# Optimization experiments

Hardware: AMD Instinct MI355X
Metric: run time of the kernel (lower is better)

The kernel has to match this reference:

```python
import jax, jax.numpy as jnp
import numpy as np

IN_FEATURES = 512
OUT_FEATURES = 128
KERNEL_DIM = 32
BATCH = 128


def setup_inputs() -> dict:
    key = jax.random.key(0)
    kx, kT = jax.random.split(key)
    x = jax.random.normal(kx, (BATCH, IN_FEATURES), dtype=jnp.float32)
    # nn.Parameter initialized with normal(0, 1)
    T = jax.random.normal(kT, (IN_FEATURES, OUT_FEATURES, KERNEL_DIM), dtype=jnp.float32)
    return {"x": x, "T": T}


def reference(x, T):
    B = x.shape[0]
    in_f, out_f, k_dim = T.shape
    # projection: [B, in] @ [in, out*k] -> [B, out, k]
    m = (x @ T.reshape(in_f, out_f * k_dim)).reshape(B, out_f, k_dim)
    # pairwise L1 distance over kernel dim: [B, B, out]
    # original: M = m[None], M_T = m[:, None]; norm = |M - M_T|.sum(3); o_b = exp(-norm).sum(0) - 1
    norm = jnp.abs(m[None, :, :, :] - m[:, None, :, :]).sum(axis=-1)  # [i=B, j=B, out]
    o_b = jnp.exp(-norm).sum(axis=0) - 1.0  # [B, out] (subtract self-distance term exp(0)=1)
    return jnp.concatenate([x, o_b], axis=1)  # [B, in + out]
```

## Files before the change

### kernel.cpp

```cpp
#include <hip/hip_runtime.h>

#define IN_F    512
#define NC      4096
#define OUT_COLS 640
#define AS_PITCH 136
#define MO_PITCH 36
#define BK      128

typedef __attribute__((ext_vector_type(8))) short  bf16x8;
typedef __attribute__((ext_vector_type(4))) float  f32x4;

static __device__ __forceinline__ unsigned short f2bfu(float f) {
    return (unsigned short)(__float_as_uint(f) >> 16);
}
static __device__ __forceinline__ unsigned int pack2(float lo, float hi) {
    return (__float_as_uint(lo) >> 16) | (__float_as_uint(hi) & 0xFFFF0000u);
}

__global__ __launch_bounds__(1024, 4) void fused_kernel(
    const float* __restrict__ x,
    const float* __restrict__ T,
    float* __restrict__ out)
{
    __shared__ __align__(16) char smem[51968];
    unsigned short* as = (unsigned short*)smem;
    unsigned short* bs = (unsigned short*)(smem + 34816);
    float* mo   = (float*)smem;
    float* psum = (float*)(smem + 43520);

    const int tid   = threadIdx.x;
    const int lane  = tid & 63;
    const int w     = tid >> 6;
    const int col   = lane & 15;
    const int q     = lane >> 4;
    const int o     = blockIdx.x >> 1;
    const int jhalf = blockIdx.x & 1;
    const int mt    = w >> 1;
    const int nt    = w & 1;

    if (tid < 64) {
        int idx = blockIdx.x * 64 + tid;
        int b = idx >> 7, c4 = idx & 127;
        float4 v = ((const float4*)x)[idx];
        *(float4*)(out + b * OUT_COLS + c4 * 4) = v;
    }

    f32x4 acc = {0.f, 0.f, 0.f, 0.f};
    for (int k0 = 0; k0 < IN_F; k0 += BK) {
        __syncthreads();
        #pragma unroll
        for (int p = 0; p < 4; ++p) {
            int u   = tid + p * 1024;
            int row = u >> 5, c4 = u & 31;
            float4 v = *(const float4*)(x + row * IN_F + k0 + c4 * 4);
            uint2 pv;
            pv.x = pack2(v.x, v.y); pv.y = pack2(v.z, v.w);
            *(uint2*)(as + row * AS_PITCH + c4 * 4) = pv;
        }
        {
            int kk = tid >> 3, cq = tid & 7;
            float4 v = *(const float4*)(T + (size_t)(k0 + kk) * NC + o * 32 + cq * 4);
            int nb = cq * 4;
            bs[(nb + 0) * AS_PITCH + kk] = f2bfu(v.x);
            bs[(nb + 1) * AS_PITCH + kk] = f2bfu(v.y);
            bs[(nb + 2) * AS_PITCH + kk] = f2bfu(v.z);
            bs[(nb + 3) * AS_PITCH + kk] = f2bfu(v.w);
        }
        __syncthreads();
        #pragma unroll
        for (int kt = 0; kt < 4; ++kt) {
            const int krel = kt * 32 + q * 8;
            bf16x8 af  = *(const bf16x8*)(as + (mt * 16 + col) * AS_PITCH + krel);
            bf16x8 bfr = *(const bf16x8*)(bs + (nt * 16 + col) * AS_PITCH + krel);
            acc = __builtin_amdgcn_mfma_f32_16x16x32_bf16(af, bfr, acc, 0, 0, 0);
        }
    }
    __syncthreads();
    {
        float* dst = mo + (size_t)(mt * 16 + q * 4) * MO_PITCH + nt * 16 + col;
        dst[0 * MO_PITCH] = acc[0]; dst[1 * MO_PITCH] = acc[1];
        dst[2 * MO_PITCH] = acc[2]; dst[3 * MO_PITCH] = acc[3];
    }
    __syncthreads();

    const int jj5 = tid & 31;
    const int isl = tid >> 5;
    const int j0  = jhalf * 64 + jj5;

    float mj0[32], mj1[32];
    #pragma unroll
    for (int k4 = 0; k4 < 8; ++k4) {
        float4 a = *(const float4*)(mo + (size_t)j0 * MO_PITCH + k4 * 4);
        float4 b = *(const float4*)(mo + (size_t)(j0 + 32) * MO_PITCH + k4 * 4);
        mj0[k4*4+0] = a.x; mj0[k4*4+1] = a.y; mj0[k4*4+2] = a.z; mj0[k4*4+3] = a.w;
        mj1[k4*4+0] = b.x; mj1[k4*4+1] = b.y; mj1[k4*4+2] = b.z; mj1[k4*4+3] = b.w;
    }

    float s0 = 0.f, s1 = 0.f;
    #pragma unroll
    for (int ii = 0; ii < 4; ++ii) {
        const int i = isl * 4 + ii;
        float n0 = 0.f, n1 = 0.f;
        #pragma unroll
        for (int k4 = 0; k4 < 8; ++k4) {
            float4 v = *(const float4*)(mo + (size_t)i * MO_PITCH + k4 * 4);
            n0 += fabsf(mj0[k4*4+0] - v.x) + fabsf(mj0[k4*4+1] - v.y)
                + fabsf(mj0[k4*4+2] - v.z) + fabsf(mj0[k4*4+3] - v.w);
            n1 += fabsf(mj1[k4*4+0] - v.x) + fabsf(mj1[k4*4+1] - v.y)
                + fabsf(mj1[k4*4+2] - v.z) + fabsf(mj1[k4*4+3] - v.w);
        }
        s0 += __expf(-n0);
        s1 += __expf(-n1);
    }
    psum[jj5 * 33 + isl]        = s0;
    psum[1056 + jj5 * 33 + isl] = s1;
    __syncthreads();
    if (tid < 64) {
        int jsel = tid >> 5, jj = tid & 31;
        float tot = 0.f;
        #pragma unroll
        for (int u = 0; u < 32; ++u) tot += psum[jsel * 1056 + jj * 33 + u];
        out[(jhalf * 64 + jsel * 32 + jj) * OUT_COLS + IN_F + o] = tot - 1.0f;
    }
}

extern "C" void kernel_launch(void* const* d_in, const int* in_sizes, int n_in,
                              void* d_out, int out_size, void* d_ws, size_t ws_size,
                              hipStream_t stream) {
    const float* x = (const float*)d_in[0];
    const float* T = (const float*)d_in[1];
    float* out = (float*)d_out;
    (void)d_ws; (void)ws_size;

    fused_kernel<<<256, 1024, 0, stream>>>(x, T, out);
}
```

Baseline: 75.98 us.

## Pre-pack x into MFMA fragment layout in a prep kernel, load T once

A new prep kernel copies x into the output and converts x to bf16 in the exact per-lane MFMA fragment order, writing it to workspace. The fused kernel then reads A fragments straight from global memory (L2-shared across the 256 blocks). It stages its whole T slice into LDS once, already in fragment order, instead of looping over four K-chunks with barriers. This removes the redundant per-block conversion of all of x and most of the syncs, at the cost of a second launch and a global round trip for the packed x.

```diff
diff --git a/kernel.cpp b/kernel.cpp
--- a/kernel.cpp
+++ b/kernel.cpp
@@ -3,9 +3,9 @@
 #define IN_F    512
 #define NC      4096
 #define OUT_COLS 640
-#define AS_PITCH 136
+#define B_SZ    128
+#define KD      32
 #define MO_PITCH 36
-#define BK      128
 
 typedef __attribute__((ext_vector_type(8))) short  bf16x8;
 typedef __attribute__((ext_vector_type(4))) float  f32x4;
@@ -17,16 +17,32 @@
     return (__float_as_uint(lo) >> 16) | (__float_as_uint(hi) & 0xFFFF0000u);
 }
 
+__global__ __launch_bounds__(256) void prep_kernel(
+    const float* __restrict__ x, float* __restrict__ out,
+    unsigned short* __restrict__ xa)
+{
+    const int g = blockIdx.x * 256 + threadIdx.x;
+    {
+        int b = g >> 7, c4 = g & 127;
+        float4 v = ((const float4*)x)[g];
+        *(float4*)(out + b * OUT_COLS + c4 * 4) = v;
+    }
+    const int s = g >> 1, half = g & 1;
+    const int mt = s >> 10, kt = (s >> 6) & 15, lane = s & 63;
+    const int col = lane & 15, q = lane >> 4;
+    float4 v = *(const float4*)(x + (mt * 16 + col) * IN_F + kt * 32 + q * 8 + half * 4);
+    uint2 pv; pv.x = pack2(v.x, v.y); pv.y = pack2(v.z, v.w);
+    *(uint2*)(xa + (size_t)s * 8 + half * 4) = pv;
+}
+
 __global__ __launch_bounds__(1024, 4) void fused_kernel(
-    const float* __restrict__ x,
+    const unsigned short* __restrict__ xa,
     const float* __restrict__ T,
     float* __restrict__ out)
 {
-    __shared__ __align__(16) char smem[51968];
-    unsigned short* as = (unsigned short*)smem;
-    unsigned short* bs = (unsigned short*)(smem + 34816);
-    float* mo   = (float*)smem;
-    float* psum = (float*)(smem + 43520);
+    __shared__ unsigned short bs[2 * 16 * 64 * 8];
+    __shared__ float mo[B_SZ * MO_PITCH];
+    __shared__ float psum[2 * 32 * 33];
 
     const int tid   = threadIdx.x;
     const int lane  = tid & 63;
@@ -35,47 +51,33 @@
     const int q     = lane >> 4;
     const int o     = blockIdx.x >> 1;
     const int jhalf = blockIdx.x & 1;
-    const int mt    = w >> 1;
-    const int nt    = w & 1;
+    const int mt    = w >> 1, nt = w & 1;
 
-    if (tid < 64) {
-        int idx = blockIdx.x * 64 + tid;
-        int b = idx >> 7, c4 = idx & 127;
-        float4 v = ((const float4*)x)[idx];
-        *(float4*)(out + b * OUT_COLS + c4 * 4) = v;
-    }
-
-    f32x4 acc = {0.f, 0.f, 0.f, 0.f};
-    for (int k0 = 0; k0 < IN_F; k0 += BK) {
-        __syncthreads();
+    #pragma unroll
+    for (int p = 0; p < 4; ++p) {
+        int u  = tid + p * 1024;
+        int kk = u >> 3, cq = u & 7;
+        float4 v = *(const float4*)(T + (size_t)kk * NC + o * 32 + cq * 4);
+        int kt = kk >> 5, qq = (kk >> 3) & 3, j = kk & 7;
+        float e[4] = {v.x, v.y, v.z, v.w};
         #pragma unroll
-        for (int p = 0; p < 4; ++p) {
-            int u   = tid + p * 1024;
-            int row = u >> 5, c4 = u & 31;
-            float4 v = *(const float4*)(x + row * IN_F + k0 + c4 * 4);
-            uint2 pv;
-            pv.x = pack2(v.x, v.y); pv.y = pack2(v.z, v.w);
-            *(uint2*)(as + row * AS_PITCH + c4 * 4) = pv;
-        }
-        {
-            int kk = tid >> 3, cq = tid & 7;
-            float4 v = *(const float4*)(T + (size_t)(k0 + kk) * NC + o * 32 + cq * 4);
-            int nb = cq * 4;
-            bs[(nb + 0) * AS_PITCH + kk] = f2bfu(v.x);
-            bs[(nb + 1) * AS_PITCH + kk] = f2bfu(v.y);
-            bs[(nb + 2) * AS_PITCH + kk] = f2bfu(v.z);
-            bs[(nb + 3) * AS_PITCH + kk] = f2bfu(v.w);
-        }
-        __syncthreads();
-        #pragma unroll
-        for (int kt = 0; kt < 4; ++kt) {
-            const int krel = kt * 32 + q * 8;
-            bf16x8 af  = *(const bf16x8*)(as + (mt * 16 + col) * AS_PITCH + krel);
-            bf16x8 bfr = *(const bf16x8*)(bs + (nt * 16 + col) * AS_PITCH + krel);
-            acc = __builtin_amdgcn_mfma_f32_16x16x32_bf16(af, bfr, acc, 0, 0, 0);
+        for (int r = 0; r < 4; ++r) {
+            int nn = cq * 4 + r;
+            int ln = qq * 16 + (nn & 15);
+            bs[((((nn >> 4) * 16 + kt) * 64) + ln) * 8 + j] = f2bfu(e[r]);
         }
     }
     __syncthreads();
+
+    f32x4 acc = {0.f, 0.f, 0.f, 0.f};
+    const unsigned short* pa = xa + ((size_t)(mt * 16) * 64 + lane) * 8;
+    const unsigned short* pb = bs + ((size_t)(nt * 16) * 64 + lane) * 8;
+    #pragma unroll 4
+    for (int kt = 0; kt < 16; ++kt) {
+        bf16x8 af  = *(const bf16x8*)(pa + (size_t)kt * 512);
+        bf16x8 bfr = *(const bf16x8*)(pb + (size_t)kt * 512);
+        acc = __builtin_amdgcn_mfma_f32_16x16x32_bf16(af, bfr, acc, 0, 0, 0);
+    }
     {
         float* dst = mo + (size_t)(mt * 16 + q * 4) * MO_PITCH + nt * 16 + col;
         dst[0 * MO_PITCH] = acc[0]; dst[1 * MO_PITCH] = acc[1];
@@ -87,7 +89,7 @@
     const int isl = tid >> 5;
     const int j0  = jhalf * 64 + jj5;
 
-    float mj0[32], mj1[32];
+    float mj0[KD], mj1[KD];
     #pragma unroll
     for (int k4 = 0; k4 < 8; ++k4) {
         float4 a = *(const float4*)(mo + (size_t)j0 * MO_PITCH + k4 * 4);
@@ -130,7 +132,8 @@
     const float* x = (const float*)d_in[0];
     const float* T = (const float*)d_in[1];
     float* out = (float*)d_out;
-    (void)d_ws; (void)ws_size;
+    unsigned short* xa = (unsigned short*)d_ws;
 
-    fused_kernel<<<256, 1024, 0, stream>>>(x, T, out);
+    prep_kernel<<<64, 256, 0, stream>>>(x, out, xa);
+    fused_kernel<<<256, 1024, 0, stream>>>(xa, T, out);
 }
```

Result: faster. 71.06 us (-6.5%).
